# Optimization experiments

Hardware: AMD Instinct MI355X
Metric: run time of the kernel (lower is better)

## Reference

```python
import jax, jax.numpy as jnp
import numpy as np

DELTA = 1.0


def _gravity_step(c, t, delta):
    # c: [B, N, 3]
    centroid = jnp.mean(c, axis=1, keepdims=True)            # [B, 1, 3]
    directions = centroid - c                                # [B, N, 3]
    dist = jnp.linalg.norm(directions, axis=-1)              # [B, N]
    directions = directions / dist[..., None]                # unit vectors
    extent = jnp.max(c, axis=1) - jnp.min(c, axis=1)         # [B, 3]
    m = jnp.prod(extent, axis=-1) ** (1.0 / 3.0)             # [B]
    d2 = jnp.square((dist - delta) * t) / (2.0 * m[:, None]) # [B, N]
    return c + d2[..., None] * directions


def setup_inputs() -> dict:
    key = jax.random.key(0)
    B, N = 8, 2_000_000
    coordinates = jax.random.normal(key, (B, N, 3), dtype=jnp.float32)
    return {
        "coordinates": coordinates,
        "t": jnp.float32(1.0),
        "iterations": 5,
    }


def reference(coordinates, t, iterations):
    c = coordinates
    for _ in range(iterations):
        c = _gravity_step(c, t, DELTA)
    return c
```

## Files before the change

kernel.cpp:

```cpp
#include <hip/hip_runtime.h>
#include <float.h>
#include <math.h>


#define NBATCH 8
#define PART_STRIDE 16
#define SLOTS_PER_BATCH 2048

__device__ __forceinline__ void block_reduce9(
    float& sx, float& sy, float& sz,
    float& mnx, float& mny, float& mnz,
    float& mxx, float& mxy, float& mxz,
    float (*red)[9]) {
#pragma unroll
  for (int off = 32; off > 0; off >>= 1) {
    sx += __shfl_down(sx, off);
    sy += __shfl_down(sy, off);
    sz += __shfl_down(sz, off);
    mnx = fminf(mnx, __shfl_down(mnx, off));
    mny = fminf(mny, __shfl_down(mny, off));
    mnz = fminf(mnz, __shfl_down(mnz, off));
    mxx = fmaxf(mxx, __shfl_down(mxx, off));
    mxy = fmaxf(mxy, __shfl_down(mxy, off));
    mxz = fmaxf(mxz, __shfl_down(mxz, off));
  }
  const int lane = threadIdx.x & 63;
  const int wave = threadIdx.x >> 6;
  if (lane == 0) {
    red[wave][0] = sx;  red[wave][1] = sy;  red[wave][2] = sz;
    red[wave][3] = mnx; red[wave][4] = mny; red[wave][5] = mnz;
    red[wave][6] = mxx; red[wave][7] = mxy; red[wave][8] = mxz;
  }
  __syncthreads();
  if (threadIdx.x == 0) {
#pragma unroll
    for (int w = 1; w < 4; ++w) {
      sx += red[w][0]; sy += red[w][1]; sz += red[w][2];
      mnx = fminf(mnx, red[w][3]); mny = fminf(mny, red[w][4]); mnz = fminf(mnz, red[w][5]);
      mxx = fmaxf(mxx, red[w][6]); mxy = fmaxf(mxy, red[w][7]); mxz = fmaxf(mxz, red[w][8]);
    }
  }
}

template <bool UPDATE, bool ACC>
__global__ __launch_bounds__(256)
void gravity_step_kernel(const float4* __restrict__ in, float4* __restrict__ out,
                         const float4* __restrict__ params,
                         float* __restrict__ partials, int N) {
  const int batch = blockIdx.y;
  const int p0 = (blockIdx.x * 256 + (int)threadIdx.x) * 4;

  float4 prm = make_float4(0.f, 0.f, 0.f, 0.f);
  if (UPDATE) prm = params[batch];

  float sx = 0.f, sy = 0.f, sz = 0.f;
  float mnx = FLT_MAX, mny = FLT_MAX, mnz = FLT_MAX;
  float mxx = -FLT_MAX, mxy = -FLT_MAX, mxz = -FLT_MAX;

  if (p0 < N) {
    const int fb = batch * ((N >> 2) * 3) + (p0 >> 2) * 3;
    float4 a = in[fb], b = in[fb + 1], g = in[fb + 2];
#define DO_POINT(X, Y, Z)                                                \
    do {                                                                 \
      if (UPDATE) {                                                      \
        float dx = prm.x - (X), dy = prm.y - (Y), dz = prm.z - (Z);      \
        float r2 = dx * dx + dy * dy + dz * dz;                          \
        float rd = rsqrtf(r2);                                           \
        float dm = r2 * rd - 1.0f;                         \
        float k = prm.w * dm * dm * rd;                                  \
        (X) += k * dx; (Y) += k * dy; (Z) += k * dz;                     \
      }                                                                  \
      if (ACC) {                                                         \
        sx += (X); sy += (Y); sz += (Z);                                 \
        mnx = fminf(mnx, (X)); mny = fminf(mny, (Y)); mnz = fminf(mnz, (Z)); \
        mxx = fmaxf(mxx, (X)); mxy = fmaxf(mxy, (Y)); mxz = fmaxf(mxz, (Z)); \
      }                                                                  \
    } while (0)

    DO_POINT(a.x, a.y, a.z);
    DO_POINT(a.w, b.x, b.y);
    DO_POINT(b.z, b.w, g.x);
    DO_POINT(g.y, g.z, g.w);
#undef DO_POINT

    if (UPDATE) {
      out[fb] = a; out[fb + 1] = b; out[fb + 2] = g;
    }
  }

  if (ACC) {
    __shared__ float red[4][9];
    block_reduce9(sx, sy, sz, mnx, mny, mnz, mxx, mxy, mxz, red);
    if (threadIdx.x == 0) {
      float4* p = (float4*)(partials +
                            (batch * SLOTS_PER_BATCH + blockIdx.x) * PART_STRIDE);
      p[0] = make_float4(sx, sy, sz, mnx);
      p[1] = make_float4(mny, mnz, mxx, mxy);
      p[2] = make_float4(mxz, 0.f, 0.f, 0.f);
    }
  }
}

__global__ __launch_bounds__(256)
void gravity_finalize_kernel(const float* __restrict__ partials,
                             const float* __restrict__ t_ptr,
                             float4* __restrict__ params, int N, int nslots) {
  const int b = blockIdx.x;
  float sx = 0.f, sy = 0.f, sz = 0.f;
  float mnx = FLT_MAX, mny = FLT_MAX, mnz = FLT_MAX;
  float mxx = -FLT_MAX, mxy = -FLT_MAX, mxz = -FLT_MAX;

  for (int s = threadIdx.x; s < nslots; s += 256) {
    const float4* p =
        (const float4*)(partials + (b * SLOTS_PER_BATCH + s) * PART_STRIDE);
    float4 q0 = p[0], q1 = p[1], q2 = p[2];
    sx += q0.x; sy += q0.y; sz += q0.z;
    mnx = fminf(mnx, q0.w); mny = fminf(mny, q1.x); mnz = fminf(mnz, q1.y);
    mxx = fmaxf(mxx, q1.z); mxy = fmaxf(mxy, q1.w); mxz = fmaxf(mxz, q2.x);
  }

  __shared__ float red[4][9];
  block_reduce9(sx, sy, sz, mnx, mny, mnz, mxx, mxy, mxz, red);

  if (threadIdx.x == 0) {
    const float invN = 1.0f / (float)N;
    float cx = sx * invN, cy = sy * invN, cz = sz * invN;
    float ex = mxx - mnx, ey = mxy - mny, ez = mxz - mnz;
    float m = cbrtf(ex * ey * ez);
    float t = *t_ptr;
    params[b] = make_float4(cx, cy, cz, t * t / (2.0f * m));
  }
}

extern "C" void kernel_launch(void* const* d_in, const int* in_sizes, int n_in,
                              void* d_out, int out_size, void* d_ws, size_t ws_size,
                              hipStream_t stream) {
  const float4* in4 = (const float4*)d_in[0];
  const float* t_ptr = (const float*)d_in[1];
  float4* out4 = (float4*)d_out;

  const int N = in_sizes[0] / (NBATCH * 3);
  const int nblk = (N + 1023) / 1024;

  float* partials = (float*)d_ws;
  float4* params =
      (float4*)((char*)d_ws + NBATCH * SLOTS_PER_BATCH * PART_STRIDE * sizeof(float));

  const dim3 grid((unsigned)nblk, NBATCH);
  const dim3 block(256);

  gravity_step_kernel<false, true><<<grid, block, 0, stream>>>(
      in4, nullptr, nullptr, partials, N);
  gravity_finalize_kernel<<<dim3(NBATCH), block, 0, stream>>>(
      partials, t_ptr, params, N, nblk);

  const float4* src = in4;
  for (int i = 0; i < 5; ++i) {
    if (i < 4) {
      gravity_step_kernel<true, true><<<grid, block, 0, stream>>>(
          src, out4, params + i * NBATCH, partials, N);
      gravity_finalize_kernel<<<dim3(NBATCH), block, 0, stream>>>(
          partials, t_ptr, params + (i + 1) * NBATCH, N, nblk);
    } else {
      gravity_step_kernel<true, false><<<grid, block, 0, stream>>>(
          src, out4, params + i * NBATCH, nullptr, N);
    }
    src = out4;
  }
}
```

Measured before the change: 674.6 us.

## Fuse all gravity iterations into one persistent cooperative kernel with grid syncs

Replaces the chain of per-iteration step and finalize launches with a single cooperative kernel using a fixed grid of 128 blocks per batch. Each block streams chunks in a grid-stride loop, commits per-block stats into double-buffered partials, and after grid.sync every block reduces the partials itself to get the centroid and scale. This removes kernel launch gaps and the separate finalize kernels. The cost is lower occupancy from the persistent grid and grid-wide barriers, and the old path is kept as a fallback if the cooperative launch fails.

```diff
diff --git a/kernel.cpp b/kernel.cpp
--- a/kernel.cpp
+++ b/kernel.cpp
@@ -1,11 +1,15 @@
 #include <hip/hip_runtime.h>
+#include <hip/hip_cooperative_groups.h>
 #include <float.h>
 #include <math.h>
 
+namespace cg = cooperative_groups;
+
 
 #define NBATCH 8
+#define GPB 128
 #define PART_STRIDE 16
-#define SLOTS_PER_BATCH 2048
+
 
 __device__ __forceinline__ void block_reduce9(
     float& sx, float& sy, float& sz,
@@ -42,6 +46,137 @@
   }
 }
 
+
+template <bool UPDATE, bool ACC>
+__device__ __forceinline__ void stream_pass(
+    const float4* __restrict__ src, float4* __restrict__ dst, float4 prm,
+    int batch_f4, int nchunks, int bx, int N,
+    float& sx, float& sy, float& sz,
+    float& mnx, float& mny, float& mnz,
+    float& mxx, float& mxy, float& mxz) {
+  sx = sy = sz = 0.f;
+  mnx = mny = mnz = FLT_MAX;
+  mxx = mxy = mxz = -FLT_MAX;
+  for (int ch = bx; ch < nchunks; ch += GPB) {
+    const int p0 = (ch * 256 + (int)threadIdx.x) * 4;
+    if (p0 < N) {
+      const int fb = batch_f4 + (p0 >> 2) * 3;
+      float4 a = src[fb], b = src[fb + 1], g = src[fb + 2];
+#define DO_POINT(X, Y, Z)                                                \
+      do {                                                               \
+        if (UPDATE) {                                                    \
+          float dx = prm.x - (X), dy = prm.y - (Y), dz = prm.z - (Z);    \
+          float r2 = dx * dx + dy * dy + dz * dz;                        \
+          float rd = rsqrtf(r2);                                         \
+          float dm = r2 * rd - 1.0f;                       \
+          float k = prm.w * dm * dm * rd;                                \
+          (X) += k * dx; (Y) += k * dy; (Z) += k * dz;                   \
+        }                                                                \
+        if (ACC) {                                                       \
+          sx += (X); sy += (Y); sz += (Z);                               \
+          mnx = fminf(mnx, (X)); mny = fminf(mny, (Y)); mnz = fminf(mnz, (Z)); \
+          mxx = fmaxf(mxx, (X)); mxy = fmaxf(mxy, (Y)); mxz = fmaxf(mxz, (Z)); \
+        }                                                                \
+      } while (0)
+      DO_POINT(a.x, a.y, a.z);
+      DO_POINT(a.w, b.x, b.y);
+      DO_POINT(b.z, b.w, g.x);
+      DO_POINT(g.y, g.z, g.w);
+#undef DO_POINT
+      if (UPDATE) {
+        dst[fb] = a; dst[fb + 1] = b; dst[fb + 2] = g;
+      }
+    }
+  }
+}
+
+__device__ __forceinline__ void commit_stats(
+    float* __restrict__ partials, int parity, int batch, int bx,
+    float sx, float sy, float sz,
+    float mnx, float mny, float mnz,
+    float mxx, float mxy, float mxz,
+    float (*red)[9]) {
+  block_reduce9(sx, sy, sz, mnx, mny, mnz, mxx, mxy, mxz, red);
+  if (threadIdx.x == 0) {
+    float4* p = (float4*)(partials +
+                          ((size_t)((parity * NBATCH + batch) * GPB + bx)) * PART_STRIDE);
+    p[0] = make_float4(sx, sy, sz, mnx);
+    p[1] = make_float4(mny, mnz, mxx, mxy);
+    p[2] = make_float4(mxz, 0.f, 0.f, 0.f);
+  }
+}
+
+__device__ __forceinline__ float4 reduce_params(
+    const float* __restrict__ partials, int parity, int batch,
+    const float* __restrict__ t_ptr, int N,
+    float (*red)[9], float4* prm_sh) {
+  float sx = 0.f, sy = 0.f, sz = 0.f;
+  float mnx = FLT_MAX, mny = FLT_MAX, mnz = FLT_MAX;
+  float mxx = -FLT_MAX, mxy = -FLT_MAX, mxz = -FLT_MAX;
+  if (threadIdx.x < GPB) {
+    const float4* p = (const float4*)(partials +
+        ((size_t)((parity * NBATCH + batch) * GPB + (int)threadIdx.x)) * PART_STRIDE);
+    float4 q0 = p[0], q1 = p[1], q2 = p[2];
+    sx = q0.x; sy = q0.y; sz = q0.z;
+    mnx = q0.w; mny = q1.x; mnz = q1.y;
+    mxx = q1.z; mxy = q1.w; mxz = q2.x;
+  }
+  block_reduce9(sx, sy, sz, mnx, mny, mnz, mxx, mxy, mxz, red);
+  if (threadIdx.x == 0) {
+    const float invN = 1.0f / (float)N;
+    float cx = sx * invN, cy = sy * invN, cz = sz * invN;
+    float ex = mxx - mnx, ey = mxy - mny, ez = mxz - mnz;
+    float m = cbrtf(ex * ey * ez);
+    float t = *t_ptr;
+    *prm_sh = make_float4(cx, cy, cz, t * t / (2.0f * m));
+  }
+  __syncthreads();
+  return *prm_sh;
+}
+
+__global__ __launch_bounds__(256, 4)
+void gravity_fused_kernel(const float4* __restrict__ in, float4* __restrict__ out,
+                          const float* __restrict__ t_ptr,
+                          float* __restrict__ partials, int N) {
+  cg::grid_group grid = cg::this_grid();
+  const int batch = blockIdx.y;
+  const int bx = blockIdx.x;
+  const int nchunks = (N + 1023) >> 10;
+  const int batch_f4 = batch * ((N >> 2) * 3);
+
+  __shared__ float red[4][9];
+  __shared__ float4 prm_sh;
+
+  float sx, sy, sz, mnx, mny, mnz, mxx, mxy, mxz;
+
+  stream_pass<false, true>(in, nullptr, make_float4(0.f, 0.f, 0.f, 0.f),
+                           batch_f4, nchunks, bx, N,
+                           sx, sy, sz, mnx, mny, mnz, mxx, mxy, mxz);
+  commit_stats(partials, 0, batch, bx, sx, sy, sz, mnx, mny, mnz, mxx, mxy, mxz, red);
+  grid.sync();
+  float4 prm = reduce_params(partials, 0, batch, t_ptr, N, red, &prm_sh);
+
+  const float4* src = in;
+  for (int it = 0; it < 5; ++it) {
+    if (it < 4) {
+      stream_pass<true, true>(src, out, prm, batch_f4, nchunks, bx, N,
+                              sx, sy, sz, mnx, mny, mnz, mxx, mxy, mxz);
+      const int par = (it + 1) & 1;
+      commit_stats(partials, par, batch, bx,
+                   sx, sy, sz, mnx, mny, mnz, mxx, mxy, mxz, red);
+      grid.sync();
+      prm = reduce_params(partials, par, batch, t_ptr, N, red, &prm_sh);
+    } else {
+      stream_pass<true, false>(src, out, prm, batch_f4, nchunks, bx, N,
+                               sx, sy, sz, mnx, mny, mnz, mxx, mxy, mxz);
+    }
+    src = out;
+  }
+}
+
+
+#define FB_SLOTS_PER_BATCH 2048
+
 template <bool UPDATE, bool ACC>
 __global__ __launch_bounds__(256)
 void gravity_step_kernel(const float4* __restrict__ in, float4* __restrict__ out,
@@ -53,9 +188,10 @@
   float4 prm = make_float4(0.f, 0.f, 0.f, 0.f);
   if (UPDATE) prm = params[batch];
 
-  float sx = 0.f, sy = 0.f, sz = 0.f;
-  float mnx = FLT_MAX, mny = FLT_MAX, mnz = FLT_MAX;
-  float mxx = -FLT_MAX, mxy = -FLT_MAX, mxz = -FLT_MAX;
+  float sx, sy, sz, mnx, mny, mnz, mxx, mxy, mxz;
+  sx = sy = sz = 0.f;
+  mnx = mny = mnz = FLT_MAX;
+  mxx = mxy = mxz = -FLT_MAX;
 
   if (p0 < N) {
     const int fb = batch * ((N >> 2) * 3) + (p0 >> 2) * 3;
@@ -66,7 +202,7 @@
         float dx = prm.x - (X), dy = prm.y - (Y), dz = prm.z - (Z);      \
         float r2 = dx * dx + dy * dy + dz * dz;                          \
         float rd = rsqrtf(r2);                                           \
-        float dm = r2 * rd - 1.0f;                         \
+        float dm = r2 * rd - 1.0f;                                       \
         float k = prm.w * dm * dm * rd;                                  \
         (X) += k * dx; (Y) += k * dy; (Z) += k * dz;                     \
       }                                                                  \
@@ -76,13 +212,11 @@
         mxx = fmaxf(mxx, (X)); mxy = fmaxf(mxy, (Y)); mxz = fmaxf(mxz, (Z)); \
       }                                                                  \
     } while (0)
-
     DO_POINT(a.x, a.y, a.z);
     DO_POINT(a.w, b.x, b.y);
     DO_POINT(b.z, b.w, g.x);
     DO_POINT(g.y, g.z, g.w);
 #undef DO_POINT
-
     if (UPDATE) {
       out[fb] = a; out[fb + 1] = b; out[fb + 2] = g;
     }
@@ -93,7 +227,7 @@
     block_reduce9(sx, sy, sz, mnx, mny, mnz, mxx, mxy, mxz, red);
     if (threadIdx.x == 0) {
       float4* p = (float4*)(partials +
-                            (batch * SLOTS_PER_BATCH + blockIdx.x) * PART_STRIDE);
+                            (size_t)(batch * FB_SLOTS_PER_BATCH + blockIdx.x) * PART_STRIDE);
       p[0] = make_float4(sx, sy, sz, mnx);
       p[1] = make_float4(mny, mnz, mxx, mxy);
       p[2] = make_float4(mxz, 0.f, 0.f, 0.f);
@@ -111,8 +245,8 @@
   float mxx = -FLT_MAX, mxy = -FLT_MAX, mxz = -FLT_MAX;
 
   for (int s = threadIdx.x; s < nslots; s += 256) {
-    const float4* p =
-        (const float4*)(partials + (b * SLOTS_PER_BATCH + s) * PART_STRIDE);
+    const float4* p = (const float4*)(partials +
+        (size_t)(b * FB_SLOTS_PER_BATCH + s) * PART_STRIDE);
     float4 q0 = p[0], q1 = p[1], q2 = p[2];
     sx += q0.x; sy += q0.y; sz += q0.z;
     mnx = fminf(mnx, q0.w); mny = fminf(mny, q1.x); mnz = fminf(mnz, q1.y);
@@ -132,6 +266,7 @@
   }
 }
 
+
 extern "C" void kernel_launch(void* const* d_in, const int* in_sizes, int n_in,
                               void* d_out, int out_size, void* d_ws, size_t ws_size,
                               hipStream_t stream) {
@@ -140,27 +275,41 @@
   float4* out4 = (float4*)d_out;
 
   const int N = in_sizes[0] / (NBATCH * 3);
+
+  float* partials = (float*)d_ws;
+
+  {
+    dim3 cgrid(GPB, NBATCH);
+    dim3 cblock(256);
+    int n_arg = N;
+    void* args[] = {(void*)&in4, (void*)&out4, (void*)&t_ptr,
+                    (void*)&partials, (void*)&n_arg};
+    hipError_t e = hipLaunchCooperativeKernel(
+        reinterpret_cast<void*>(gravity_fused_kernel), cgrid, cblock, args, 0, stream);
+    if (e == hipSuccess) return;
+    (void)hipGetLastError();
+  }
+
   const int nblk = (N + 1023) / 1024;
-
-  float* partials = (float*)d_ws;
+  float* fb_partials = (float*)d_ws;
   float4* params =
-      (float4*)((char*)d_ws + NBATCH * SLOTS_PER_BATCH * PART_STRIDE * sizeof(float));
+      (float4*)((char*)d_ws + (size_t)NBATCH * FB_SLOTS_PER_BATCH * PART_STRIDE * sizeof(float));
 
   const dim3 grid((unsigned)nblk, NBATCH);
   const dim3 block(256);
 
   gravity_step_kernel<false, true><<<grid, block, 0, stream>>>(
-      in4, nullptr, nullptr, partials, N);
+      in4, nullptr, nullptr, fb_partials, N);
   gravity_finalize_kernel<<<dim3(NBATCH), block, 0, stream>>>(
-      partials, t_ptr, params, N, nblk);
+      fb_partials, t_ptr, params, N, nblk);
 
   const float4* src = in4;
   for (int i = 0; i < 5; ++i) {
     if (i < 4) {
       gravity_step_kernel<true, true><<<grid, block, 0, stream>>>(
-          src, out4, params + i * NBATCH, partials, N);
+          src, out4, params + i * NBATCH, fb_partials, N);
       gravity_finalize_kernel<<<dim3(NBATCH), block, 0, stream>>>(
-          partials, t_ptr, params + (i + 1) * NBATCH, N, nblk);
+          fb_partials, t_ptr, params + (i + 1) * NBATCH, N, nblk);
     } else {
       gravity_step_kernel<true, false><<<grid, block, 0, stream>>>(
           src, out4, params + i * NBATCH, nullptr, N);
```

New measurement: 1.401 ms. +107.6%, slower.
